# Performance work log

Measured on AMD Instinct MI355X. Metric: run time of the kernel, lower is better.

The kernel has to match this reference:

```python
import jax, jax.numpy as jnp
import numpy as np

B, L, K, D = 32, 1024, 1024, 1024

def setup_inputs() -> dict:
    key = jax.random.key(0)
    k1, k2, k3, k4, k5 = jax.random.split(key, 5)
    query = jax.random.normal(k1, (B, L, D), dtype=jnp.float32)
    context = jax.random.normal(k2, (B, K, D), dtype=jnp.float32)
    mask = jax.random.randint(k3, (B * L, K), 0, 2, dtype=jnp.int32)
    W_in = jax.random.normal(k4, (D, D), dtype=jnp.float32) * (D ** -0.5)
    W_out = jax.random.normal(k5, (D, 2 * D), dtype=jnp.float32) * ((2 * D) ** -0.5)
    return {"query": query, "context": context, "mask": mask, "W_in": W_in, "W_out": W_out}

def reference(query, context, mask, W_in, W_out):
    b, l, d = query.shape
    k = context.shape[1]
    # linear_in (general attention): q @ W_in.T
    q = jnp.einsum('bld,ed->ble', query, W_in)
    # attention scores [b, l, k]
    scores = jnp.einsum('bld,bkd->blk', q, context)
    # multiplicative-mask softmax with renormalization (masked_softmax, non-memory-efficient path)
    m = mask.astype(scores.dtype).reshape(b, l, k)
    w = jax.nn.softmax(scores * m, axis=-1) * m
    w = w / (jnp.sum(w, axis=-1, keepdims=True) + 1e-13)
    # mix attended context, concat with transformed query, project, tanh
    mix = jnp.einsum('blk,bkd->bld', w, context)
    combined = jnp.concatenate([mix, q], axis=-1)          # [b, l, 2d]
    out = jnp.tanh(jnp.einsum('blc,dc->bld', combined, W_out))
    return out
```

## Files before the change

### kernel.cpp

```cpp
#include <hip/hip_runtime.h>
#include <math.h>

typedef __bf16 bf16_t;
typedef __bf16 bf16x4 __attribute__((ext_vector_type(4)));
typedef __bf16 bf16x8 __attribute__((ext_vector_type(8)));
typedef _Float16 f16x4 __attribute__((ext_vector_type(4)));
typedef _Float16 f16x8 __attribute__((ext_vector_type(8)));
typedef float f32x4 __attribute__((ext_vector_type(4)));

#define MFMA_BF16 __builtin_amdgcn_mfma_f32_16x16x32_bf16
#define MFMA_F16  __builtin_amdgcn_mfma_f32_16x16x32_f16


__device__ __forceinline__ bf16_t to_bf16_rne(float x, float& rep) {
    unsigned u = __builtin_bit_cast(unsigned, x);
    unsigned r = u + 0x7fffu + ((u >> 16) & 1u);
    unsigned short h = (unsigned short)(r >> 16);
    rep = __builtin_bit_cast(float, ((unsigned)h) << 16);
    return __builtin_bit_cast(bf16_t, h);
}

__device__ __forceinline__ void g2l16(const void* g, void* l) {
    __builtin_amdgcn_global_load_lds(
        (const __attribute__((address_space(1))) unsigned int*)g,
        (__attribute__((address_space(3))) unsigned int*)l, 16, 0, 0);
}

__device__ __forceinline__ int lch(int r, int j) {
    return (r * 8 + (j ^ (r & 7))) * 8;
}

template <typename T>
__device__ __forceinline__ void stage2(const T* __restrict__ gA, long long ldA,
                                       const T* __restrict__ gB, long long ldB,
                                       T* buf, int tid) {
    int wid = tid >> 6, lane = tid & 63;
#pragma unroll
    for (int i = 0; i < 4; ++i) {
        int cb = i * 512 + wid * 64;
        int c = cb + lane;
        int r = c >> 3, j = (c & 7) ^ (r & 7);
        g2l16(gA + (long long)r * ldA + j * 8, buf + (size_t)cb * 8);
    }
#pragma unroll
    for (int i = 0; i < 4; ++i) {
        int cb = i * 512 + wid * 64;
        int c = cb + lane;
        int r = c >> 3, j = (c & 7) ^ (r & 7);
        g2l16(gB + (long long)r * ldB + j * 8, buf + 16384 + (size_t)cb * 8);
    }
}


__global__ __launch_bounds__(256) void split_int_k(const float* __restrict__ in,
                                                   bf16_t* __restrict__ out,
                                                   long long n4) {
    long long i = (long long)blockIdx.x * 256 + threadIdx.x;
    if (i >= n4) return;
    f32x4 v = ((const f32x4*)in)[i];
    bf16x4 hv, lv;
#pragma unroll
    for (int j = 0; j < 4; ++j) {
        float rep;
        hv[j] = to_bf16_rne(v[j], rep);
        float res = v[j] - rep;
        float rep2;
        lv[j] = to_bf16_rne(res, rep2);
    }
    long long row = i >> 8;
    int k = (int)(i & 255) * 4;
    long long base = row * 2048 + ((k >> 5) << 6) + (k & 31);
    *(bf16x4*)(out + base) = hv;
    *(bf16x4*)(out + base + 32) = lv;
}

__global__ __launch_bounds__(256) void cast_f16_k(const float* __restrict__ in,
                                                  _Float16* __restrict__ o, long long n4) {
    long long i = (long long)blockIdx.x * 256 + threadIdx.x;
    if (i >= n4) return;
    f32x4 v = ((const f32x4*)in)[i];
    f16x4 h;
#pragma unroll
    for (int j = 0; j < 4; ++j) h[j] = (_Float16)v[j];
    ((f16x4*)o)[i] = h;
}

__global__ __launch_bounds__(256) void transpose_ctx_k(const float* __restrict__ ctx,
                                                       _Float16* __restrict__ ctxT) {
    __shared__ _Float16 t[32][34];
    int b = blockIdx.z;
    int k0 = blockIdx.x * 32, d0 = blockIdx.y * 32;
    const float* src = ctx + ((long long)b * 1024 + k0) * 1024 + d0;
#pragma unroll
    for (int i = 0; i < 4; ++i) {
        int y = threadIdx.y + i * 8;
        t[y][threadIdx.x] = (_Float16)src[(long long)y * 1024 + threadIdx.x];
    }
    __syncthreads();
    _Float16* dst = ctxT + ((long long)b * 1024 + d0) * 1024 + k0;
#pragma unroll
    for (int i = 0; i < 4; ++i) {
        int y = threadIdx.y + i * 8;
        dst[(long long)y * 1024 + threadIdx.x] = t[threadIdx.x][y];
    }
}

__global__ __launch_bounds__(256) void masked_softmax_k(const float* __restrict__ s,
                                                        const int* __restrict__ m,
                                                        _Float16* __restrict__ w) {
    long long row = blockIdx.x;
    const float* sr = s + row * 1024;
    const int* mr = m + row * 1024;
    _Float16* wr_ = w + row * 1024;
    int t = threadIdx.x;
    int lane = t & 63, wid = t >> 6;
    float v[4];
    int mk[4];
    float mx = -3.0e38f;
#pragma unroll
    for (int i = 0; i < 4; ++i) {
        int idx = t + i * 256;
        v[i] = sr[idx];
        mk[i] = mr[idx];
        if (mk[i]) mx = fmaxf(mx, v[i]);
    }
#pragma unroll
    for (int off = 32; off; off >>= 1) mx = fmaxf(mx, __shfl_xor(mx, off));
    __shared__ float rm[4], rs[4];
    if (!lane) rm[wid] = mx;
    __syncthreads();
    mx = fmaxf(fmaxf(rm[0], rm[1]), fmaxf(rm[2], rm[3]));
    float sum = 0.f;
#pragma unroll
    for (int i = 0; i < 4; ++i) {
        float e = mk[i] ? expf(v[i] - mx) : 0.f;
        v[i] = e;
        sum += e;
    }
#pragma unroll
    for (int off = 32; off; off >>= 1) sum += __shfl_xor(sum, off);
    if (!lane) rs[wid] = sum;
    __syncthreads();
    sum = rs[0] + rs[1] + rs[2] + rs[3];
    float inv = sum > 0.f ? 1.0f / sum : 0.f;
#pragma unroll
    for (int i = 0; i < 4; ++i) wr_[t + i * 256] = (_Float16)(v[i] * inv);
}

template <int EPI>
__global__ __launch_bounds__(512, 2) void gemm_x3_256(
    const bf16_t* __restrict__ Aint, const bf16_t* __restrict__ Bint,
    long long sA, long long sB, long long sC, int nbx, int nby,
    float* __restrict__ Cs, bf16_t* __restrict__ Qint, _Float16* __restrict__ Qf) {
    __shared__ bf16_t lds[65536];
    const int NT = 32;
    int tid = threadIdx.x, lane = tid & 63, wid = tid >> 6;
    int wr = wid >> 2, wc = wid & 3;
    int nwg = gridDim.x;
    int bid = blockIdx.x;
    int lid = (bid & 7) * (nwg >> 3) + (bid >> 3);
    int by = lid % nby;
    int t2 = lid / nby;
    int bx = t2 % nbx;
    int z = t2 / nbx;
    const bf16_t* At = Aint + (long long)z * sA + (long long)bx * 256 * 2048;
    const bf16_t* Bt = Bint + (long long)z * sB + (long long)by * 256 * 2048;
    stage2(At, 2048ll, Bt, 2048ll, lds, tid);
    stage2(At + 64, 2048ll, Bt + 64, 2048ll, lds + 32768, tid);
    f32x4 acc[8][4] = {};
    for (int t = 0; t < NT; ++t) {
        bf16_t* buf = lds + (size_t)(t & 1) * 32768;
        bf16_t* bufB = buf + 16384;
        if (t < NT - 1) {
            asm volatile("s_waitcnt vmcnt(8)" ::: "memory");
        } else {
            asm volatile("s_waitcnt vmcnt(0)" ::: "memory");
        }
        __builtin_amdgcn_sched_barrier(0);
        __builtin_amdgcn_s_barrier();
        __builtin_amdgcn_sched_barrier(0);
        bf16x8 bh[4], bl[4];
#pragma unroll
        for (int n = 0; n < 4; ++n) {
            int rB = wc * 64 + n * 16 + (lane & 15);
            bh[n] = *(const bf16x8*)(bufB + lch(rB, lane >> 4));
            bl[n] = *(const bf16x8*)(bufB + lch(rB, 4 + (lane >> 4)));
        }
#pragma unroll
        for (int p = 0; p < 3; ++p) {
            bf16x8 ah[2], al[2];
#pragma unroll
            for (int i = 0; i < 2; ++i) {
                int rA = wr * 128 + (p * 2 + i) * 16 + (lane & 15);
                ah[i] = *(const bf16x8*)(buf + lch(rA, lane >> 4));
                al[i] = *(const bf16x8*)(buf + lch(rA, 4 + (lane >> 4)));
            }
            __builtin_amdgcn_s_setprio(1);
#pragma unroll
            for (int i = 0; i < 2; ++i)
#pragma unroll
                for (int n = 0; n < 4; ++n) {
                    f32x4 a = acc[p * 2 + i][n];
                    a = MFMA_BF16(ah[i], bh[n], a, 0, 0, 0);
                    a = MFMA_BF16(ah[i], bl[n], a, 0, 0, 0);
                    a = MFMA_BF16(al[i], bh[n], a, 0, 0, 0);
                    acc[p * 2 + i][n] = a;
                }
            __builtin_amdgcn_s_setprio(0);
        }
        bf16x8 ah3[2], al3[2];
#pragma unroll
        for (int i = 0; i < 2; ++i) {
            int rA = wr * 128 + (6 + i) * 16 + (lane & 15);
            ah3[i] = *(const bf16x8*)(buf + lch(rA, lane >> 4));
            al3[i] = *(const bf16x8*)(buf + lch(rA, 4 + (lane >> 4)));
        }
        asm volatile("s_waitcnt lgkmcnt(0)" ::: "memory");
        __builtin_amdgcn_sched_barrier(0);
        __builtin_amdgcn_s_barrier();
        __builtin_amdgcn_sched_barrier(0);
        if (t + 2 < NT)
            stage2(At + (long long)(t + 2) * 64, 2048ll, Bt + (long long)(t + 2) * 64,
                   2048ll, buf, tid);
        __builtin_amdgcn_s_setprio(1);
#pragma unroll
        for (int i = 0; i < 2; ++i)
#pragma unroll
            for (int n = 0; n < 4; ++n) {
                f32x4 a = acc[6 + i][n];
                a = MFMA_BF16(ah3[i], bh[n], a, 0, 0, 0);
                a = MFMA_BF16(ah3[i], bl[n], a, 0, 0, 0);
                a = MFMA_BF16(al3[i], bh[n], a, 0, 0, 0);
                acc[6 + i][n] = a;
            }
        __builtin_amdgcn_s_setprio(0);
    }
    int r0 = bx * 256 + wr * 128 + ((lane >> 4) << 2);
    int c0 = by * 256 + wc * 64 + (lane & 15);
#pragma unroll
    for (int m = 0; m < 8; ++m)
#pragma unroll
        for (int n = 0; n < 4; ++n)
#pragma unroll
            for (int j = 0; j < 4; ++j) {
                int r = r0 + m * 16 + j;
                int c = c0 + n * 16;
                float v = acc[m][n][j];
                if (EPI == 0) {
                    Cs[(long long)z * sC + (long long)r * 1024 + c] = v;
                } else {
                    float rep;
                    bf16_t hb = to_bf16_rne(v, rep);
                    float res = v - rep;
                    float rep2;
                    bf16_t lb = to_bf16_rne(res, rep2);
                    long long rb = (long long)r * 2048 + ((c >> 5) << 6) + (c & 31);
                    Qint[rb] = hb;
                    Qint[rb + 32] = lb;
                    Qf[(long long)r * 1024 + c] = (_Float16)v;
                }
            }
}

template <int EPI>
__global__ __launch_bounds__(512, 2) void gemm_f16_256(
    const _Float16* __restrict__ A1, const _Float16* __restrict__ A2,
    const _Float16* __restrict__ B,
    long long ldA, long long ldB, long long sA, long long sB, long long sC,
    int NT, int swt, int nbx, int nby,
    _Float16* __restrict__ Cm, float* __restrict__ Co) {
    __shared__ _Float16 lds[65536];
    int tid = threadIdx.x, lane = tid & 63, wid = tid >> 6;
    int wr = wid >> 2, wc = wid & 3;
    int nwg = gridDim.x;
    int bid = blockIdx.x;
    int lid = (bid & 7) * (nwg >> 3) + (bid >> 3);
    int by = lid % nby;
    int t2 = lid / nby;
    int bx = t2 % nbx;
    int z = t2 / nbx;
    const _Float16* A1t = A1 + (long long)z * sA + (long long)bx * 256 * ldA;
    const _Float16* A2t = A2 + (long long)bx * 256 * ldA;
    const _Float16* Bt = B + (long long)z * sB + (long long)by * 256 * ldB;
    stage2((0 < swt) ? A1t : A2t, ldA, Bt, ldB, lds, tid);
    stage2((1 < swt) ? A1t + 64 : A2t + (long long)(1 - swt) * 64, ldA, Bt + 64, ldB,
           lds + 32768, tid);
    f32x4 acc[8][4] = {};
    for (int t = 0; t < NT; ++t) {
        _Float16* buf = lds + (size_t)(t & 1) * 32768;
        _Float16* bufB = buf + 16384;
        if (t < NT - 1) {
            asm volatile("s_waitcnt vmcnt(8)" ::: "memory");
        } else {
            asm volatile("s_waitcnt vmcnt(0)" ::: "memory");
        }
        __builtin_amdgcn_sched_barrier(0);
        __builtin_amdgcn_s_barrier();
        __builtin_amdgcn_sched_barrier(0);
        f16x8 bfr[4][2];
#pragma unroll
        for (int n = 0; n < 4; ++n)
#pragma unroll
            for (int ks = 0; ks < 2; ++ks) {
                int rB = wc * 64 + n * 16 + (lane & 15);
                bfr[n][ks] = *(const f16x8*)(bufB + lch(rB, ks * 4 + (lane >> 4)));
            }
#pragma unroll
        for (int p = 0; p < 3; ++p) {
            f16x8 a[2][2];
#pragma unroll
            for (int i = 0; i < 2; ++i)
#pragma unroll
                for (int ks = 0; ks < 2; ++ks) {
                    int rA = wr * 128 + (p * 2 + i) * 16 + (lane & 15);
                    a[i][ks] = *(const f16x8*)(buf + lch(rA, ks * 4 + (lane >> 4)));
                }
            __builtin_amdgcn_s_setprio(1);
#pragma unroll
            for (int i = 0; i < 2; ++i)
#pragma unroll
                for (int n = 0; n < 4; ++n) {
                    f32x4 v = acc[p * 2 + i][n];
                    v = MFMA_F16(a[i][0], bfr[n][0], v, 0, 0, 0);
                    v = MFMA_F16(a[i][1], bfr[n][1], v, 0, 0, 0);
                    acc[p * 2 + i][n] = v;
                }
            __builtin_amdgcn_s_setprio(0);
        }
        f16x8 a3[2][2];
#pragma unroll
        for (int i = 0; i < 2; ++i)
#pragma unroll
            for (int ks = 0; ks < 2; ++ks) {
                int rA = wr * 128 + (6 + i) * 16 + (lane & 15);
                a3[i][ks] = *(const f16x8*)(buf + lch(rA, ks * 4 + (lane >> 4)));
            }
        asm volatile("s_waitcnt lgkmcnt(0)" ::: "memory");
        __builtin_amdgcn_sched_barrier(0);
        __builtin_amdgcn_s_barrier();
        __builtin_amdgcn_sched_barrier(0);
        if (t + 2 < NT) {
            int tt = t + 2;
            const _Float16* gA =
                (tt < swt) ? A1t + (long long)tt * 64 : A2t + (long long)(tt - swt) * 64;
            stage2(gA, ldA, Bt + (long long)tt * 64, ldB, buf, tid);
        }
        __builtin_amdgcn_s_setprio(1);
#pragma unroll
        for (int i = 0; i < 2; ++i)
#pragma unroll
            for (int n = 0; n < 4; ++n) {
                f32x4 v = acc[6 + i][n];
                v = MFMA_F16(a3[i][0], bfr[n][0], v, 0, 0, 0);
                v = MFMA_F16(a3[i][1], bfr[n][1], v, 0, 0, 0);
                acc[6 + i][n] = v;
            }
        __builtin_amdgcn_s_setprio(0);
    }
    int r0 = bx * 256 + wr * 128 + ((lane >> 4) << 2);
    int c0 = by * 256 + wc * 64 + (lane & 15);
#pragma unroll
    for (int m = 0; m < 8; ++m)
#pragma unroll
        for (int n = 0; n < 4; ++n)
#pragma unroll
            for (int j = 0; j < 4; ++j) {
                int r = r0 + m * 16 + j;
                int c = c0 + n * 16;
                float v = acc[m][n][j];
                if (EPI == 0) {
                    Cm[(long long)z * sC + (long long)r * 1024 + c] = (_Float16)v;
                } else {
                    Co[(long long)r * 1024 + c] = tanhf(v);
                }
            }
}


extern "C" void kernel_launch(void* const* d_in, const int* in_sizes, int n_in,
                              void* d_out, int out_size, void* d_ws, size_t ws_size,
                              hipStream_t stream) {
    const float* query = (const float*)d_in[0];
    const float* ctx = (const float*)d_in[1];
    const int* mask = (const int*)d_in[2];
    const float* Win = (const float*)d_in[3];
    const float* Wout = (const float*)d_in[4];
    float* outp = (float*)d_out;

    const long long MB = 1048576ll;
    int G = 1;
    if ((long long)ws_size >= 648 * MB) G = 32;
    else if ((long long)ws_size >= 328 * MB) G = 16;
    else if ((long long)ws_size >= 168 * MB) G = 8;
    else if ((long long)ws_size >= 88 * MB) G = 4;
    else if ((long long)ws_size >= 48 * MB) G = 2;

    char* p = (char*)d_ws;
    bf16_t* win_int = (bf16_t*)p; p += 4 * MB;
    _Float16* woutf = (_Float16*)p; p += 4 * MB;
    const long long R = (long long)G * 1024;
    bf16_t* qint = (bf16_t*)p; p += 4 * G * MB;
    _Float16* qf = (_Float16*)p; p += 2 * G * MB;
    bf16_t* ctx_int = (bf16_t*)p; p += 4 * G * MB;
    _Float16* ctxT = (_Float16*)p; p += 2 * G * MB;
    _Float16* wf = (_Float16*)p; p += 2 * G * MB;
    _Float16* mixf = (_Float16*)p; p += 2 * G * MB;
    bf16_t* qs_int = (bf16_t*)p;
    float* scores = (float*)p;

    const long long LD = 1048576ll;

    split_int_k<<<1024, 256, 0, stream>>>(Win, win_int, 262144ll);
    cast_f16_k<<<2048, 256, 0, stream>>>(Wout, woutf, 524288ll);

    for (int b0 = 0; b0 < 32; b0 += G) {
        const float* qsrc = query + (long long)b0 * LD;
        const float* csrc = ctx + (long long)b0 * LD;
        split_int_k<<<(int)R, 256, 0, stream>>>(qsrc, qs_int, R * 256);
        gemm_x3_256<1><<<16 * G, 512, 0, stream>>>(
            qs_int, win_int, 0, 0, 0, 4 * G, 4, nullptr, qint, qf);
        split_int_k<<<(int)R, 256, 0, stream>>>(csrc, ctx_int, R * 256);
        transpose_ctx_k<<<dim3(32, 32, G), dim3(32, 8, 1), 0, stream>>>(csrc, ctxT);
        gemm_x3_256<0><<<16 * G, 512, 0, stream>>>(
            qint, ctx_int, 2097152ll, 2097152ll, 1048576ll, 4, 4,
            scores, nullptr, nullptr);
        masked_softmax_k<<<(int)R, 256, 0, stream>>>(
            scores, mask + (long long)b0 * 1024 * 1024, wf);
        gemm_f16_256<0><<<16 * G, 512, 0, stream>>>(
            wf, wf, ctxT, 1024ll, 1024ll, 1048576ll, 1048576ll, 1048576ll,
            16, 1 << 20, 4, 4, mixf, nullptr);
        gemm_f16_256<1><<<16 * G, 512, 0, stream>>>(
            mixf, qf, woutf, 1024ll, 2048ll, 0, 0, 0,
            32, 16, 4 * G, 4, nullptr, outp + (long long)b0 * LD);
    }
}
```

Baseline: 784.4 us.

## Fuse context split with transpose, vectorize softmax, alias workspace slabs

```diff
diff --git a/kernel.cpp b/kernel.cpp
--- a/kernel.cpp
+++ b/kernel.cpp
@@ -7,6 +7,7 @@
 typedef _Float16 f16x4 __attribute__((ext_vector_type(4)));
 typedef _Float16 f16x8 __attribute__((ext_vector_type(8)));
 typedef float f32x4 __attribute__((ext_vector_type(4)));
+typedef int i32x4 __attribute__((ext_vector_type(4)));
 
 #define MFMA_BF16 __builtin_amdgcn_mfma_f32_16x16x32_bf16
 #define MFMA_F16  __builtin_amdgcn_mfma_f32_16x16x32_f16
@@ -85,23 +86,33 @@
     ((f16x4*)o)[i] = h;
 }
 
-__global__ __launch_bounds__(256) void transpose_ctx_k(const float* __restrict__ ctx,
-                                                       _Float16* __restrict__ ctxT) {
-    __shared__ _Float16 t[32][34];
+__global__ __launch_bounds__(256) void prep_ctx_k(const float* __restrict__ ctx,
+                                                  bf16_t* __restrict__ ctx_int,
+                                                  _Float16* __restrict__ ctxT) {
+    __shared__ _Float16 tl[32][33];
     int b = blockIdx.z;
     int k0 = blockIdx.x * 32, d0 = blockIdx.y * 32;
     const float* src = ctx + ((long long)b * 1024 + k0) * 1024 + d0;
+    int x = threadIdx.x, y = threadIdx.y;
 #pragma unroll
     for (int i = 0; i < 4; ++i) {
-        int y = threadIdx.y + i * 8;
-        t[y][threadIdx.x] = (_Float16)src[(long long)y * 1024 + threadIdx.x];
+        int k = y + i * 8;
+        float v = src[(long long)k * 1024 + x];
+        float rep;
+        bf16_t hb = to_bf16_rne(v, rep);
+        float rep2;
+        bf16_t lb = to_bf16_rne(v - rep, rep2);
+        long long rb = ((long long)b * 1024 + k0 + k) * 2048 + d0 * 2 + x;
+        ctx_int[rb] = hb;
+        ctx_int[rb + 32] = lb;
+        tl[x][k] = (_Float16)v;
     }
     __syncthreads();
     _Float16* dst = ctxT + ((long long)b * 1024 + d0) * 1024 + k0;
 #pragma unroll
     for (int i = 0; i < 4; ++i) {
-        int y = threadIdx.y + i * 8;
-        dst[(long long)y * 1024 + threadIdx.x] = t[threadIdx.x][y];
+        int dd = y + i * 8;
+        dst[(long long)dd * 1024 + x] = tl[dd][x];
     }
 }
 
@@ -109,21 +120,17 @@
                                                         const int* __restrict__ m,
                                                         _Float16* __restrict__ w) {
     long long row = blockIdx.x;
-    const float* sr = s + row * 1024;
-    const int* mr = m + row * 1024;
-    _Float16* wr_ = w + row * 1024;
+    const f32x4* sr = (const f32x4*)(s + row * 1024);
+    const i32x4* mr = (const i32x4*)(m + row * 1024);
+    f16x4* wr_ = (f16x4*)(w + row * 1024);
     int t = threadIdx.x;
     int lane = t & 63, wid = t >> 6;
-    float v[4];
-    int mk[4];
+    f32x4 v = sr[t];
+    i32x4 mk = mr[t];
     float mx = -3.0e38f;
 #pragma unroll
-    for (int i = 0; i < 4; ++i) {
-        int idx = t + i * 256;
-        v[i] = sr[idx];
-        mk[i] = mr[idx];
+    for (int i = 0; i < 4; ++i)
         if (mk[i]) mx = fmaxf(mx, v[i]);
-    }
 #pragma unroll
     for (int off = 32; off; off >>= 1) mx = fmaxf(mx, __shfl_xor(mx, off));
     __shared__ float rm[4], rs[4];
@@ -131,11 +138,11 @@
     __syncthreads();
     mx = fmaxf(fmaxf(rm[0], rm[1]), fmaxf(rm[2], rm[3]));
     float sum = 0.f;
+    f32x4 e;
 #pragma unroll
     for (int i = 0; i < 4; ++i) {
-        float e = mk[i] ? expf(v[i] - mx) : 0.f;
-        v[i] = e;
-        sum += e;
+        e[i] = mk[i] ? expf(v[i] - mx) : 0.f;
+        sum += e[i];
     }
 #pragma unroll
     for (int off = 32; off; off >>= 1) sum += __shfl_xor(sum, off);
@@ -143,8 +150,10 @@
     __syncthreads();
     sum = rs[0] + rs[1] + rs[2] + rs[3];
     float inv = sum > 0.f ? 1.0f / sum : 0.f;
-#pragma unroll
-    for (int i = 0; i < 4; ++i) wr_[t + i * 256] = (_Float16)(v[i] * inv);
+    f16x4 o;
+#pragma unroll
+    for (int i = 0; i < 4; ++i) o[i] = (_Float16)(e[i] * inv);
+    wr_[t] = o;
 }
 
 template <int EPI>
@@ -343,7 +352,8 @@
             int tt = t + 2;
             const _Float16* gA =
                 (tt < swt) ? A1t + (long long)tt * 64 : A2t + (long long)(tt - swt) * 64;
-            stage2(gA, ldA, Bt + (long long)tt * 64, ldB, buf, tid);
+            stage2(gA, ldA, Bt + (long long)tt * 64, ldB,
+                   lds + (size_t)(tt & 1) * 32768, tid);
         }
         __builtin_amdgcn_s_setprio(1);
 #pragma unroll
@@ -389,43 +399,43 @@
 
     const long long MB = 1048576ll;
     int G = 1;
-    if ((long long)ws_size >= 648 * MB) G = 32;
-    else if ((long long)ws_size >= 328 * MB) G = 16;
-    else if ((long long)ws_size >= 168 * MB) G = 8;
-    else if ((long long)ws_size >= 88 * MB) G = 4;
-    else if ((long long)ws_size >= 48 * MB) G = 2;
+    if ((long long)ws_size >= 512 * MB) G = 32;
+    else if ((long long)ws_size >= 256 * MB) G = 16;
+    else if ((long long)ws_size >= 128 * MB) G = 8;
+    else if ((long long)ws_size >= 64 * MB) G = 4;
+    else if ((long long)ws_size >= 32 * MB) G = 2;
 
     char* p = (char*)d_ws;
-    bf16_t* win_int = (bf16_t*)p; p += 4 * MB;
-    _Float16* woutf = (_Float16*)p; p += 4 * MB;
     const long long R = (long long)G * 1024;
     bf16_t* qint = (bf16_t*)p; p += 4 * G * MB;
     _Float16* qf = (_Float16*)p; p += 2 * G * MB;
-    bf16_t* ctx_int = (bf16_t*)p; p += 4 * G * MB;
+    char* slabA = p; p += 4 * G * MB;
+    bf16_t* win_int = (bf16_t*)slabA;
+    bf16_t* ctx_int = (bf16_t*)slabA;
+    _Float16* wf = (_Float16*)slabA;
+    _Float16* mixf = (_Float16*)(slabA + 2 * G * MB);
     _Float16* ctxT = (_Float16*)p; p += 2 * G * MB;
-    _Float16* wf = (_Float16*)p; p += 2 * G * MB;
-    _Float16* mixf = (_Float16*)p; p += 2 * G * MB;
-    bf16_t* qs_int = (bf16_t*)p;
-    float* scores = (float*)p;
+    char* slabC = p;
+    bf16_t* qs_int = (bf16_t*)slabC;
+    float* scores = (float*)slabC;
+    _Float16* woutf = (_Float16*)slabC;
 
     const long long LD = 1048576ll;
-
-    split_int_k<<<1024, 256, 0, stream>>>(Win, win_int, 262144ll);
-    cast_f16_k<<<2048, 256, 0, stream>>>(Wout, woutf, 524288ll);
 
     for (int b0 = 0; b0 < 32; b0 += G) {
         const float* qsrc = query + (long long)b0 * LD;
         const float* csrc = ctx + (long long)b0 * LD;
+        split_int_k<<<1024, 256, 0, stream>>>(Win, win_int, 262144ll);
         split_int_k<<<(int)R, 256, 0, stream>>>(qsrc, qs_int, R * 256);
         gemm_x3_256<1><<<16 * G, 512, 0, stream>>>(
             qs_int, win_int, 0, 0, 0, 4 * G, 4, nullptr, qint, qf);
-        split_int_k<<<(int)R, 256, 0, stream>>>(csrc, ctx_int, R * 256);
-        transpose_ctx_k<<<dim3(32, 32, G), dim3(32, 8, 1), 0, stream>>>(csrc, ctxT);
+        prep_ctx_k<<<dim3(32, 32, G), dim3(32, 8, 1), 0, stream>>>(csrc, ctx_int, ctxT);
         gemm_x3_256<0><<<16 * G, 512, 0, stream>>>(
             qint, ctx_int, 2097152ll, 2097152ll, 1048576ll, 4, 4,
             scores, nullptr, nullptr);
         masked_softmax_k<<<(int)R, 256, 0, stream>>>(
             scores, mask + (long long)b0 * 1024 * 1024, wf);
+        cast_f16_k<<<2048, 256, 0, stream>>>(Wout, woutf, 524288ll);
         gemm_f16_256<0><<<16 * G, 512, 0, stream>>>(
             wf, wf, ctxT, 1024ll, 1024ll, 1048576ll, 1048576ll, 1048576ll,
             16, 1 << 20, 4, 4, mixf, nullptr);
```

Result: no change. 778.8 us (-0.7%).
